# Kernel tuning notes

Hardware: AMD Instinct MI355X
Metric: run time of the kernel (lower is better)

Reference implementation:

```python
import jax, jax.numpy as jnp
import numpy as np

N, XC, YC, H, W_ = 1024, 512, 256, 8, 8
HID = 512


def setup_inputs() -> dict:
    key = jax.random.key(0)
    k = jax.random.split(key, 6)
    x_samples = jax.random.normal(k[0], (N, XC, H, W_), dtype=jnp.float32)
    y_samples = jax.random.normal(k[1], (N, YC, H, W_), dtype=jnp.float32)
    # p_mu: Linear(x_dim, hidden) -> ReLU -> Linear(hidden, y_dim)
    s1 = 1.0 / np.sqrt(XC)
    s2 = 1.0 / np.sqrt(HID)
    W1 = jax.random.uniform(k[2], (XC, HID), jnp.float32, -s1, s1)
    b1 = jax.random.uniform(k[3], (HID,), jnp.float32, -s1, s1)
    W2 = jax.random.uniform(k[4], (HID, YC), jnp.float32, -s2, s2)
    b2 = jax.random.uniform(k[5], (YC,), jnp.float32, -s2, s2)
    return {"x_samples": x_samples, "y_samples": y_samples,
            "W1": W1, "b1": b1, "W2": W2, "b2": b2}


def reference(x_samples, y_samples, W1, b1, W2, b2):
    # AdaptiveAvgPool2d(1) + flatten(1) == mean over spatial dims
    x_vec = x_samples.mean(axis=(2, 3))  # (N, x_dim)
    y_vec = y_samples.mean(axis=(2, 3))  # (N, y_dim)
    # p_mu MLP
    h = jax.nn.relu(x_vec @ W1 + b1)
    mu = h @ W2 + b2  # (N, y_dim)
    # positive: -(mu_i - y_i)^2 / 2, summed over D
    positive = (-((mu - y_vec) ** 2) / 2.0).sum(axis=-1)  # (N,)
    # negative: for each i, mean_j (y_j - mu_i)^2 / 2, summed over D
    diff = y_vec[None, :, :] - mu[:, None, :]  # (N, N, D)
    negative = (-(diff ** 2).mean(axis=1) / 2.0).sum(axis=-1)  # (N,)
    return (positive - negative).mean()
```

## Files before the change

### kernel.cpp

```cpp
#include <hip/hip_runtime.h>

#define N_SAMP 1024
#define XC_DIM 512
#define YC_DIM 256
#define HID_DIM 512

__global__ __launch_bounds__(256) void pool_kernel(
    const float* __restrict__ x, const float* __restrict__ y,
    float* __restrict__ x_vec, float* __restrict__ y_vec) {
  __shared__ float s[16 * 33];
  const int t = threadIdx.x;
  const long blk = blockIdx.x;
  const float4* src;
  float* dst;
  long obase;
  if (blk < 16384) {
    src = (const float4*)x; dst = x_vec; obase = blk * 32;
  } else {
    src = (const float4*)y; dst = y_vec; obase = (blk - 16384) * 32;
  }
  const float4* p = src + obase * 16;

  float4 v0 = p[t];
  float4 v1 = p[t + 256];
  float h0 = (v0.x + v0.y) + (v0.z + v0.w);
  float h1 = (v1.x + v1.y) + (v1.z + v1.w);

  s[(t & 15) * 33 + (t >> 4)] = h0;
  s[(t & 15) * 33 + 16 + (t >> 4)] = h1;
  __syncthreads();

  const int o = t >> 3;
  const int r = t & 7;
  float dp = s[(2 * r) * 33 + o] + s[(2 * r + 1) * 33 + o];
#pragma unroll
  for (int off = 1; off < 8; off <<= 1) dp += __shfl_xor(dp, off);
  if (r == 0) dst[obase + o] = dp * (1.0f / 64.0f);
}

#define TBK 16

__global__ __launch_bounds__(256) void gemm1_kernel(
    const float* __restrict__ A, const float* __restrict__ B,
    float* __restrict__ Hp) {
  const int K = 512, Nn = 512;
  __shared__ float As[TBK][68];
  __shared__ float Bs[TBK][68];
  const int t = threadIdx.x;
  const int bn = blockIdx.x * 64;
  const int bm = blockIdx.y * 64;
  const int ks = blockIdx.z;

  const int arow = t >> 2, acol = (t & 3) * 4;
  const int brow = t >> 4, bcol = (t & 15) * 4;
  const int row0 = (t >> 4) * 4, col0 = (t & 15) * 4;

  float acc[4][4] = {};
  const int k0 = ks * 128;

  float4 av = *(const float4*)&A[(bm + arow) * K + k0 + acol];
  float4 bv = *(const float4*)&B[(k0 + brow) * Nn + bn + bcol];

  for (int it = 0; it < 8; ++it) {
    __syncthreads();
    As[acol + 0][arow] = av.x;
    As[acol + 1][arow] = av.y;
    As[acol + 2][arow] = av.z;
    As[acol + 3][arow] = av.w;
    *(float4*)&Bs[brow][bcol] = bv;
    __syncthreads();
    if (it < 7) {
      const int k1 = k0 + (it + 1) * TBK;
      av = *(const float4*)&A[(bm + arow) * K + k1 + acol];
      bv = *(const float4*)&B[(k1 + brow) * Nn + bn + bcol];
    }
#pragma unroll
    for (int kk = 0; kk < TBK; ++kk) {
      float4 a = *(const float4*)&As[kk][row0];
      float4 b = *(const float4*)&Bs[kk][col0];
      acc[0][0] += a.x * b.x; acc[0][1] += a.x * b.y; acc[0][2] += a.x * b.z; acc[0][3] += a.x * b.w;
      acc[1][0] += a.y * b.x; acc[1][1] += a.y * b.y; acc[1][2] += a.y * b.z; acc[1][3] += a.y * b.w;
      acc[2][0] += a.z * b.x; acc[2][1] += a.z * b.y; acc[2][2] += a.z * b.z; acc[2][3] += a.z * b.w;
      acc[3][0] += a.w * b.x; acc[3][1] += a.w * b.y; acc[3][2] += a.w * b.z; acc[3][3] += a.w * b.w;
    }
  }

  float* H = Hp + (long)ks * (N_SAMP * HID_DIM);
#pragma unroll
  for (int i = 0; i < 4; ++i) {
    float4 o;
    o.x = acc[i][0]; o.y = acc[i][1]; o.z = acc[i][2]; o.w = acc[i][3];
    *(float4*)&H[(long)(bm + row0 + i) * Nn + bn + col0] = o;
  }
}

__global__ __launch_bounds__(256) void gemm2_kernel(
    const float* __restrict__ Hp, const float* __restrict__ b1,
    const float* __restrict__ B, const float* __restrict__ yv,
    float* __restrict__ cs_part, float* __restrict__ ycs_part,
    float* __restrict__ dot_part) {
  const int K = 512, Nn = 256;
  __shared__ float As[TBK][68];
  __shared__ float Bs[TBK][68];
  __shared__ float redd[4];
  const int t = threadIdx.x;
  const int bn = blockIdx.x * 64;
  const int bm = blockIdx.y * 64;
  const int ks = blockIdx.z;
  const long HS = (long)N_SAMP * HID_DIM;

  const int arow = t >> 2, acol = (t & 3) * 4;
  const int brow = t >> 4, bcol = (t & 15) * 4;
  const int row0 = (t >> 4) * 4, col0 = (t & 15) * 4;

  float acc[4][4] = {};
  const int k0 = ks * 64;

  long aidx = (long)(bm + arow) * K + k0 + acol;
  float4 a0 = *(const float4*)&Hp[aidx];
  float4 a1 = *(const float4*)&Hp[aidx + HS];
  float4 a2 = *(const float4*)&Hp[aidx + 2 * HS];
  float4 a3 = *(const float4*)&Hp[aidx + 3 * HS];
  float4 bb = *(const float4*)&b1[k0 + acol];
  float4 bv = *(const float4*)&B[(k0 + brow) * Nn + bn + bcol];

  for (int it = 0; it < 4; ++it) {
    float4 av;
    av.x = fmaxf(a0.x + a1.x + a2.x + a3.x + bb.x, 0.0f);
    av.y = fmaxf(a0.y + a1.y + a2.y + a3.y + bb.y, 0.0f);
    av.z = fmaxf(a0.z + a1.z + a2.z + a3.z + bb.z, 0.0f);
    av.w = fmaxf(a0.w + a1.w + a2.w + a3.w + bb.w, 0.0f);
    __syncthreads();
    As[acol + 0][arow] = av.x;
    As[acol + 1][arow] = av.y;
    As[acol + 2][arow] = av.z;
    As[acol + 3][arow] = av.w;
    *(float4*)&Bs[brow][bcol] = bv;
    __syncthreads();
    if (it < 3) {
      const int k1 = k0 + (it + 1) * TBK;
      aidx = (long)(bm + arow) * K + k1 + acol;
      a0 = *(const float4*)&Hp[aidx];
      a1 = *(const float4*)&Hp[aidx + HS];
      a2 = *(const float4*)&Hp[aidx + 2 * HS];
      a3 = *(const float4*)&Hp[aidx + 3 * HS];
      bb = *(const float4*)&b1[k1 + acol];
      bv = *(const float4*)&B[(k1 + brow) * Nn + bn + bcol];
    }
#pragma unroll
    for (int kk = 0; kk < TBK; ++kk) {
      float4 a = *(const float4*)&As[kk][row0];
      float4 b = *(const float4*)&Bs[kk][col0];
      acc[0][0] += a.x * b.x; acc[0][1] += a.x * b.y; acc[0][2] += a.x * b.z; acc[0][3] += a.x * b.w;
      acc[1][0] += a.y * b.x; acc[1][1] += a.y * b.y; acc[1][2] += a.y * b.z; acc[1][3] += a.y * b.w;
      acc[2][0] += a.z * b.x; acc[2][1] += a.z * b.y; acc[2][2] += a.z * b.z; acc[2][3] += a.z * b.w;
      acc[3][0] += a.w * b.x; acc[3][1] += a.w * b.y; acc[3][2] += a.w * b.z; acc[3][3] += a.w * b.w;
    }
  }

  float dp = 0.f;
  float cmu0 = 0.f, cmu1 = 0.f, cmu2 = 0.f, cmu3 = 0.f;
  float cy0 = 0.f, cy1 = 0.f, cy2 = 0.f, cy3 = 0.f;
#pragma unroll
  for (int i = 0; i < 4; ++i) {
    const float4 yy = *(const float4*)&yv[(long)(bm + row0 + i) * Nn + bn + col0];
    dp += acc[i][0] * yy.x + acc[i][1] * yy.y + acc[i][2] * yy.z + acc[i][3] * yy.w;
    cmu0 += acc[i][0]; cmu1 += acc[i][1]; cmu2 += acc[i][2]; cmu3 += acc[i][3];
    cy0 += yy.x; cy1 += yy.y; cy2 += yy.z; cy3 += yy.w;
  }
#pragma unroll
  for (int off = 1; off < 64; off <<= 1) dp += __shfl_xor(dp, off);

  __syncthreads();
  {
    float4 o; o.x = cmu0; o.y = cmu1; o.z = cmu2; o.w = cmu3;
    *(float4*)&As[t >> 4][col0] = o;
    float4 q; q.x = cy0; q.y = cy1; q.z = cy2; q.w = cy3;
    *(float4*)&Bs[t >> 4][col0] = q;
  }
  if ((t & 63) == 0) redd[t >> 6] = dp;
  __syncthreads();

  const int bid = blockIdx.x + 4 * blockIdx.y + 64 * blockIdx.z;
  if (t < 64) {
    float s = 0.f;
#pragma unroll
    for (int g = 0; g < 16; ++g) s += As[g][t];
    cs_part[(blockIdx.y * 8 + ks) * 256 + bn + t] = s;
  } else if (t < 128) {
    if (ks == 0) {
      const int c = t - 64;
      float s = 0.f;
#pragma unroll
      for (int g = 0; g < 16; ++g) s += Bs[g][c];
      ycs_part[blockIdx.y * 256 + bn + c] = s;
    }
  } else if (t == 128) {
    dot_part[bid] = redd[0] + redd[1] + redd[2] + redd[3];
  }
}

__global__ __launch_bounds__(256) void finalize_kernel(
    const float* __restrict__ cs_part, const float* __restrict__ ycs_part,
    const float* __restrict__ dot_part, const float* __restrict__ b2,
    float* __restrict__ out) {
  __shared__ float red[3][4];
  const int t = threadIdx.x;
  const float b2d = b2[t];
  float cm = 1024.0f * b2d;
#pragma unroll 8
  for (int p = 0; p < 128; ++p) cm += cs_part[p * 256 + t];
  float cy = 0.f;
#pragma unroll
  for (int p = 0; p < 16; ++p) cy += ycs_part[p * 256 + t];
  float v1 = cm * cy;
  float v2 = b2d * cy;
  float v3 = dot_part[t] + dot_part[t + 256];
#pragma unroll
  for (int off = 1; off < 64; off <<= 1) {
    v1 += __shfl_xor(v1, off);
    v2 += __shfl_xor(v2, off);
    v3 += __shfl_xor(v3, off);
  }
  if ((t & 63) == 0) {
    red[0][t >> 6] = v1; red[1][t >> 6] = v2; red[2][t >> 6] = v3;
  }
  __syncthreads();
  if (t == 0) {
    float S1 = red[0][0] + red[0][1] + red[0][2] + red[0][3];
    float S2 = red[1][0] + red[1][1] + red[1][2] + red[1][3];
    float S0 = red[2][0] + red[2][1] + red[2][2] + red[2][3];
    float dot = S0 + S2;
    out[0] = dot * (1.0f / 1024.0f) - S1 * (1.0f / (1024.0f * 1024.0f));
  }
}

extern "C" void kernel_launch(void* const* d_in, const int* in_sizes, int n_in,
                              void* d_out, int out_size, void* d_ws, size_t ws_size,
                              hipStream_t stream) {
  const float* x  = (const float*)d_in[0];
  const float* y  = (const float*)d_in[1];
  const float* W1 = (const float*)d_in[2];
  const float* b1 = (const float*)d_in[3];
  const float* W2 = (const float*)d_in[4];
  const float* b2 = (const float*)d_in[5];
  float* out = (float*)d_out;

  char* ws = (char*)d_ws;
  float* x_vec = (float*)ws;
  float* y_vec = (float*)(ws + (2lu << 20));
  float* Hp    = (float*)(ws + (4lu << 20));
  float* cs_part  = (float*)(ws + (12lu << 20));
  float* ycs_part = (float*)(ws + (12lu << 20) + (160lu << 10));
  float* dot_part = (float*)(ws + (12lu << 20) + (192lu << 10));

  pool_kernel<<<24576, 256, 0, stream>>>(x, y, x_vec, y_vec);

  gemm1_kernel<<<dim3(8, 16, 4), 256, 0, stream>>>(x_vec, W1, Hp);

  gemm2_kernel<<<dim3(4, 16, 8), 256, 0, stream>>>(Hp, b1, W2, y_vec,
                                                   cs_part, ycs_part, dot_part);

  finalize_kernel<<<1, 256, 0, stream>>>(cs_part, ycs_part, dot_part, b2, out);
}
```

Baseline: 261.3 us.

## Restructure pooling to wave-per-segment loop and fuse finalize into gemm2 via counter

The pooling kernel now launches a third as many blocks. Each wave handles six 1 KB segments, covering four channels each, using shuffle reductions with no shared memory or barriers. The separate finalize kernel is removed: gemm2 blocks bump an atomic counter, and the last block performs the final reduction. The counter is reset inside the pooling kernel. This aims to cut launch overhead and per-block sync costs, at the cost of a threadfence and atomic in every gemm2 block.

```diff
diff --git a/kernel.cpp b/kernel.cpp
--- a/kernel.cpp
+++ b/kernel.cpp
@@ -4,41 +4,43 @@
 #define XC_DIM 512
 #define YC_DIM 256
 #define HID_DIM 512
+#define TBK 16
 
 __global__ __launch_bounds__(256) void pool_kernel(
     const float* __restrict__ x, const float* __restrict__ y,
-    float* __restrict__ x_vec, float* __restrict__ y_vec) {
-  __shared__ float s[16 * 33];
-  const int t = threadIdx.x;
-  const long blk = blockIdx.x;
-  const float4* src;
-  float* dst;
-  long obase;
-  if (blk < 16384) {
-    src = (const float4*)x; dst = x_vec; obase = blk * 32;
-  } else {
-    src = (const float4*)y; dst = y_vec; obase = (blk - 16384) * 32;
-  }
-  const float4* p = src + obase * 16;
-
-  float4 v0 = p[t];
-  float4 v1 = p[t + 256];
-  float h0 = (v0.x + v0.y) + (v0.z + v0.w);
-  float h1 = (v1.x + v1.y) + (v1.z + v1.w);
-
-  s[(t & 15) * 33 + (t >> 4)] = h0;
-  s[(t & 15) * 33 + 16 + (t >> 4)] = h1;
-  __syncthreads();
-
-  const int o = t >> 3;
-  const int r = t & 7;
-  float dp = s[(2 * r) * 33 + o] + s[(2 * r + 1) * 33 + o];
-#pragma unroll
-  for (int off = 1; off < 8; off <<= 1) dp += __shfl_xor(dp, off);
-  if (r == 0) dst[obase + o] = dp * (1.0f / 64.0f);
-}
-
-#define TBK 16
+    float* __restrict__ x_vec, float* __restrict__ y_vec,
+    int* __restrict__ counter) {
+  if (blockIdx.x == 0 && threadIdx.x == 0) *counter = 0;
+  const int w = blockIdx.x * 4 + (threadIdx.x >> 6);
+  const int l = threadIdx.x & 63;
+  const float4* xf = (const float4*)x;
+  const float4* yf = (const float4*)y;
+#pragma unroll
+  for (int j = 0; j < 3; ++j) {
+    const int s0 = w + (2 * j) * 32768;
+    const int s1 = w + (2 * j + 1) * 32768;
+    const float4* p0 = (s0 < 131072) ? xf + (long)s0 * 64
+                                     : yf + (long)(s0 - 131072) * 64;
+    const float4* p1 = (s1 < 131072) ? xf + (long)s1 * 64
+                                     : yf + (long)(s1 - 131072) * 64;
+    float4 v0 = p0[l];
+    float4 v1 = p1[l];
+    float h0 = (v0.x + v0.y) + (v0.z + v0.w);
+    float h1 = (v1.x + v1.y) + (v1.z + v1.w);
+    h0 += __shfl_xor(h0, 1); h1 += __shfl_xor(h1, 1);
+    h0 += __shfl_xor(h0, 2); h1 += __shfl_xor(h1, 2);
+    h0 += __shfl_xor(h0, 4); h1 += __shfl_xor(h1, 4);
+    h0 += __shfl_xor(h0, 8); h1 += __shfl_xor(h1, 8);
+    if ((l & 15) == 0) {
+      const int g0 = s0 * 4 + (l >> 4);
+      const int g1 = s1 * 4 + (l >> 4);
+      if (s0 < 131072) x_vec[g0] = h0 * (1.0f / 64.0f);
+      else             y_vec[g0 - 524288] = h0 * (1.0f / 64.0f);
+      if (s1 < 131072) x_vec[g1] = h1 * (1.0f / 64.0f);
+      else             y_vec[g1 - 524288] = h1 * (1.0f / 64.0f);
+    }
+  }
+}
 
 __global__ __launch_bounds__(256) void gemm1_kernel(
     const float* __restrict__ A, const float* __restrict__ B,
@@ -98,11 +100,14 @@
     const float* __restrict__ Hp, const float* __restrict__ b1,
     const float* __restrict__ B, const float* __restrict__ yv,
     float* __restrict__ cs_part, float* __restrict__ ycs_part,
-    float* __restrict__ dot_part) {
+    float* __restrict__ dot_part, int* __restrict__ counter,
+    const float* __restrict__ b2, float* __restrict__ out) {
   const int K = 512, Nn = 256;
   __shared__ float As[TBK][68];
   __shared__ float Bs[TBK][68];
   __shared__ float redd[4];
+  __shared__ float red2[3][4];
+  __shared__ int lastFlag;
   const int t = threadIdx.x;
   const int bn = blockIdx.x * 64;
   const int bm = blockIdx.y * 64;
@@ -198,40 +203,40 @@
   } else if (t == 128) {
     dot_part[bid] = redd[0] + redd[1] + redd[2] + redd[3];
   }
-}
-
-__global__ __launch_bounds__(256) void finalize_kernel(
-    const float* __restrict__ cs_part, const float* __restrict__ ycs_part,
-    const float* __restrict__ dot_part, const float* __restrict__ b2,
-    float* __restrict__ out) {
-  __shared__ float red[3][4];
-  const int t = threadIdx.x;
-  const float b2d = b2[t];
-  float cm = 1024.0f * b2d;
+
+  __threadfence();
+  __syncthreads();
+  if (t == 0) lastFlag = (atomicAdd(counter, 1) == 511);
+  __syncthreads();
+  if (lastFlag) {
+    __threadfence();
+    const float b2d = b2[t];
+    float cm = 1024.0f * b2d;
 #pragma unroll 8
-  for (int p = 0; p < 128; ++p) cm += cs_part[p * 256 + t];
-  float cy = 0.f;
-#pragma unroll
-  for (int p = 0; p < 16; ++p) cy += ycs_part[p * 256 + t];
-  float v1 = cm * cy;
-  float v2 = b2d * cy;
-  float v3 = dot_part[t] + dot_part[t + 256];
-#pragma unroll
-  for (int off = 1; off < 64; off <<= 1) {
-    v1 += __shfl_xor(v1, off);
-    v2 += __shfl_xor(v2, off);
-    v3 += __shfl_xor(v3, off);
-  }
-  if ((t & 63) == 0) {
-    red[0][t >> 6] = v1; red[1][t >> 6] = v2; red[2][t >> 6] = v3;
-  }
-  __syncthreads();
-  if (t == 0) {
-    float S1 = red[0][0] + red[0][1] + red[0][2] + red[0][3];
-    float S2 = red[1][0] + red[1][1] + red[1][2] + red[1][3];
-    float S0 = red[2][0] + red[2][1] + red[2][2] + red[2][3];
-    float dot = S0 + S2;
-    out[0] = dot * (1.0f / 1024.0f) - S1 * (1.0f / (1024.0f * 1024.0f));
+    for (int p = 0; p < 128; ++p) cm += cs_part[p * 256 + t];
+    float cy = 0.f;
+#pragma unroll
+    for (int p = 0; p < 16; ++p) cy += ycs_part[p * 256 + t];
+    float v1 = cm * cy;
+    float v2 = b2d * cy;
+    float v3 = dot_part[t] + dot_part[t + 256];
+#pragma unroll
+    for (int off = 1; off < 64; off <<= 1) {
+      v1 += __shfl_xor(v1, off);
+      v2 += __shfl_xor(v2, off);
+      v3 += __shfl_xor(v3, off);
+    }
+    if ((t & 63) == 0) {
+      red2[0][t >> 6] = v1; red2[1][t >> 6] = v2; red2[2][t >> 6] = v3;
+    }
+    __syncthreads();
+    if (t == 0) {
+      float S1 = red2[0][0] + red2[0][1] + red2[0][2] + red2[0][3];
+      float S2 = red2[1][0] + red2[1][1] + red2[1][2] + red2[1][3];
+      float S0 = red2[2][0] + red2[2][1] + red2[2][2] + red2[2][3];
+      float dot = S0 + S2;
+      out[0] = dot * (1.0f / 1024.0f) - S1 * (1.0f / (1024.0f * 1024.0f));
+    }
   }
 }
 
@@ -253,13 +258,13 @@
   float* cs_part  = (float*)(ws + (12lu << 20));
   float* ycs_part = (float*)(ws + (12lu << 20) + (160lu << 10));
   float* dot_part = (float*)(ws + (12lu << 20) + (192lu << 10));
-
-  pool_kernel<<<24576, 256, 0, stream>>>(x, y, x_vec, y_vec);
+  int*   counter  = (int*)  (ws + (12lu << 20) + (224lu << 10));
+
+  pool_kernel<<<8192, 256, 0, stream>>>(x, y, x_vec, y_vec, counter);
 
   gemm1_kernel<<<dim3(8, 16, 4), 256, 0, stream>>>(x_vec, W1, Hp);
 
   gemm2_kernel<<<dim3(4, 16, 8), 256, 0, stream>>>(Hp, b1, W2, y_vec,
-                                                   cs_part, ycs_part, dot_part);
-
-  finalize_kernel<<<1, 256, 0, stream>>>(cs_part, ycs_part, dot_part, b2, out);
-}
+                                                   cs_part, ycs_part, dot_part,
+                                                   counter, b2, out);
+}
```

Result: slower. 296.0 us (+13.3%).
